# Performance work log

Hardware: AMD Instinct MI355X
Metric: run time of the kernel (lower is better)

The kernel has to match this reference:

```python
import jax, jax.numpy as jnp
import numpy as np

B, H, W, C = 8, 28, 28, 1024
NH = 16
HD = C // NH
HID = 4 * C
BC = C // 2
SCALE = HD ** -0.5
EPS_LN = 1e-5   # nn.LayerNorm default
EPS_CLN = 1e-6  # detectron2 LayerNorm default


def layer_norm(x, w, b, eps=EPS_LN):
    m = jnp.mean(x, -1, keepdims=True)
    v = jnp.mean((x - m) ** 2, -1, keepdims=True)
    return (x - m) * jax.lax.rsqrt(v + eps) * w + b


def conv2d(x, w, padding):
    return jax.lax.conv_general_dilated(x, w, (1, 1), padding,
                                        dimension_numbers=("NHWC", "HWIO", "NHWC"))


def rel_table(rel_pos, size):
    # q_size == k_size, so relative index is simply (i - j) + (size - 1)
    idx = jnp.arange(size)[:, None] - jnp.arange(size)[None, :] + (size - 1)
    return rel_pos[idx]  # (size, size, HD)


def setup_inputs() -> dict:
    key = jax.random.key(0)
    ks = jax.random.split(key, 12)
    rn = lambda k, shape, s=0.02: jax.random.normal(k, shape, jnp.float32) * s
    return {
        "x": jax.random.normal(ks[0], (B, H, W, C), jnp.float32),
        "ln1_w": jnp.ones((C,), jnp.float32), "ln1_b": jnp.zeros((C,), jnp.float32),
        "qkv_w": rn(ks[1], (C, 3 * C)), "qkv_b": jnp.zeros((3 * C,), jnp.float32),
        "proj_w": rn(ks[2], (C, C)), "proj_b": jnp.zeros((C,), jnp.float32),
        "rel_pos_h": rn(ks[3], (2 * H - 1, HD)),
        "rel_pos_w": rn(ks[4], (2 * W - 1, HD)),
        "ln2_w": jnp.ones((C,), jnp.float32), "ln2_b": jnp.zeros((C,), jnp.float32),
        "mlp_w1": rn(ks[5], (C, HID)), "mlp_b1": jnp.zeros((HID,), jnp.float32),
        "mlp_w2": rn(ks[6], (HID, C)), "mlp_b2": jnp.zeros((C,), jnp.float32),
        "conv1_w": rn(ks[7], (1, 1, C, BC)),
        "cln1_w": jnp.ones((BC,), jnp.float32), "cln1_b": jnp.zeros((BC,), jnp.float32),
        "conv2_w": rn(ks[8], (3, 3, BC, BC)),
        "cln2_w": jnp.ones((BC,), jnp.float32), "cln2_b": jnp.zeros((BC,), jnp.float32),
        "conv3_w": rn(ks[9], (1, 1, BC, C)),
        "cln3_w": jnp.ones((C,), jnp.float32), "cln3_b": jnp.zeros((C,), jnp.float32),
    }


def _attention(h, qkv_w, qkv_b, proj_w, proj_b, rel_pos_h, rel_pos_w):
    # h: (B, N, C) with N = H*W
    Bq, N, _ = h.shape
    qkv = (h @ qkv_w + qkv_b).reshape(Bq, N, 3, NH, HD)
    q, k, v = jnp.moveaxis(qkv, 2, 0)          # each (B, N, NH, HD)
    q = jnp.swapaxes(q, 1, 2)                  # (B, NH, N, HD)
    k = jnp.swapaxes(k, 1, 2)
    v = jnp.swapaxes(v, 1, 2)
    attn = jnp.einsum("bhqd,bhkd->bhqk", q * SCALE, k)  # (B, NH, N, N)
    # decomposed relative position bias (uses UNscaled q, as in torch source)
    Rh = rel_table(rel_pos_h, H)               # (H, H, HD)
    Rw = rel_table(rel_pos_w, W)               # (W, W, HD)
    rq = q.reshape(Bq, NH, H, W, HD)
    rel_h = jnp.einsum("bnhwd,hkd->bnhwk", rq, Rh)  # (B, NH, H, W, H)
    rel_w = jnp.einsum("bnhwd,wkd->bnhwk", rq, Rw)  # (B, NH, H, W, W)
    attn = (attn.reshape(Bq, NH, H, W, H, W)
            + rel_h[..., :, None] + rel_w[..., None, :]).reshape(Bq, NH, N, N)
    attn = jax.nn.softmax(attn, axis=-1)
    out = jnp.einsum("bhqk,bhkd->bhqd", attn, v)     # (B, NH, N, HD)
    out = jnp.swapaxes(out, 1, 2).reshape(Bq, N, C)
    return out @ proj_w + proj_b


def reference(x, ln1_w, ln1_b, qkv_w, qkv_b, proj_w, proj_b, rel_pos_h, rel_pos_w,
              ln2_w, ln2_b, mlp_w1, mlp_b1, mlp_w2, mlp_b2,
              conv1_w, cln1_w, cln1_b, conv2_w, cln2_w, cln2_b,
              conv3_w, cln3_w, cln3_b):
    Bq = x.shape[0]
    N = H * W
    xt = x.reshape(Bq, N, C)
    shortcut = xt
    h = layer_norm(xt, ln1_w, ln1_b)
    a = _attention(h, qkv_w, qkv_b, proj_w, proj_b, rel_pos_h, rel_pos_w)
    xt = shortcut + a
    h2 = layer_norm(xt, ln2_w, ln2_b)
    mlp = jax.nn.gelu(h2 @ mlp_w1 + mlp_b1, approximate=False) @ mlp_w2 + mlp_b2
    xt = xt + mlp
    y = xt.reshape(Bq, H, W, C)
    # residual bottleneck conv block (NHWC; detectron2 LN == per-pixel channel LN)
    o = conv2d(y, conv1_w, "VALID")
    o = jax.nn.gelu(layer_norm(o, cln1_w, cln1_b, EPS_CLN), approximate=False)
    o = conv2d(o, conv2_w, "SAME")
    o = jax.nn.gelu(layer_norm(o, cln2_w, cln2_b, EPS_CLN), approximate=False)
    o = conv2d(o, conv3_w, "VALID")
    o = layer_norm(o, cln3_w, cln3_b, EPS_CLN)
    return y + o
```

## Files before the change

### kernel.cpp

```cpp
#include <hip/hip_runtime.h>
#include <hip/hip_bf16.h>

#define DI __device__ __forceinline__

typedef short bf16x8 __attribute__((ext_vector_type(8)));
typedef float f32x4 __attribute__((ext_vector_type(4)));

constexpr int BB = 8, CC = 1024, NHEAD = 16, HD = 64, HIDC = 4096, BCC = 512;
constexpr int NT = 784;
constexpr int MROWS = BB * NT;
constexpr float ATT_SCALE = 0.125f;

DI short f2bf(float f) {
    unsigned u = __builtin_bit_cast(unsigned, f);
    u = u + 0x7FFFu + ((u >> 16) & 1u);
    return (short)(u >> 16);
}
DI float bf2f(short h) {
    unsigned u = ((unsigned)(unsigned short)h) << 16;
    return __builtin_bit_cast(float, u);
}
DI float gelu_f(float x) { return 0.5f * x * (1.0f + erff(x * 0.70710678118654752f)); }

DI void gload16(const void* g, void* l) {
    __builtin_amdgcn_global_load_lds(
        (const __attribute__((address_space(1))) void*)g,
        (__attribute__((address_space(3))) void*)l, 16, 0, 0);
}

__global__ __launch_bounds__(256)
void cvt_t_kernel(const float* __restrict__ in, short* __restrict__ out, int K, int N) {
    __shared__ short t[64][68];
    const int k0 = blockIdx.y * 64, n0 = blockIdx.x * 64;
    const int tid = threadIdx.x;
    const int r = tid >> 4, c4 = (tid & 15) << 2;
    #pragma unroll
    for (int rr = 0; rr < 64; rr += 16) {
        float4 v = *(const float4*)(in + (size_t)(k0 + r + rr) * N + n0 + c4);
        t[r + rr][c4 + 0] = f2bf(v.x); t[r + rr][c4 + 1] = f2bf(v.y);
        t[r + rr][c4 + 2] = f2bf(v.z); t[r + rr][c4 + 3] = f2bf(v.w);
    }
    __syncthreads();
    #pragma unroll
    for (int rr = 0; rr < 64; rr += 16) {
        int nrow = r + rr;
        short4 o;
        o.x = t[c4 + 0][nrow]; o.y = t[c4 + 1][nrow];
        o.z = t[c4 + 2][nrow]; o.w = t[c4 + 3][nrow];
        *(short4*)(out + (size_t)(n0 + nrow) * K + k0 + c4) = o;
    }
}

__global__ void cvt_tables_kernel(const float* __restrict__ rph, const float* __restrict__ rpw,
                                  short* __restrict__ rhb, short* __restrict__ rwb) {
    int i = blockIdx.x * 256 + threadIdx.x;
    if (i < 3520) rhb[i] = f2bf(rph[i]);
    else if (i < 7040) rwb[i - 3520] = f2bf(rpw[i - 3520]);
}

template<bool GELU_, bool RESID, bool OUTBF>
__global__ void ln_kernel(const float* __restrict__ in, const float* __restrict__ gw,
                          const float* __restrict__ gb, const float* __restrict__ resid,
                          void* __restrict__ outv, int C, float eps) {
    const int row = blockIdx.x;
    const int tid = threadIdx.x;
    const float* x = in + (size_t)row * C;
    const int c4 = C >> 2;
    float s = 0.f, s2 = 0.f;
    for (int i = tid; i < c4; i += 256) {
        float4 v = ((const float4*)x)[i];
        s += v.x + v.y + v.z + v.w;
        s2 += v.x * v.x + v.y * v.y + v.z * v.z + v.w * v.w;
    }
    for (int off = 32; off; off >>= 1) { s += __shfl_xor(s, off); s2 += __shfl_xor(s2, off); }
    __shared__ float sa[4], sb[4], stats[2];
    int wid = tid >> 6;
    if ((tid & 63) == 0) { sa[wid] = s; sb[wid] = s2; }
    __syncthreads();
    if (tid == 0) {
        float S = sa[0] + sa[1] + sa[2] + sa[3];
        float S2 = sb[0] + sb[1] + sb[2] + sb[3];
        float mean = S / C;
        float var = S2 / C - mean * mean;
        stats[0] = mean; stats[1] = rsqrtf(var + eps);
    }
    __syncthreads();
    const float mean = stats[0], rstd = stats[1];
    for (int i = tid; i < c4; i += 256) {
        float4 v = ((const float4*)x)[i];
        float4 w4 = ((const float4*)gw)[i];
        float4 b4 = ((const float4*)gb)[i];
        float o[4] = { (v.x - mean) * rstd * w4.x + b4.x,
                       (v.y - mean) * rstd * w4.y + b4.y,
                       (v.z - mean) * rstd * w4.z + b4.z,
                       (v.w - mean) * rstd * w4.w + b4.w };
        if (GELU_) {
            #pragma unroll
            for (int j = 0; j < 4; j++) o[j] = gelu_f(o[j]);
        }
        if (RESID) {
            float4 r4 = ((const float4*)(resid + (size_t)row * C))[i];
            o[0] += r4.x; o[1] += r4.y; o[2] += r4.z; o[3] += r4.w;
        }
        if (OUTBF) {
            short4 ov; ov.x = f2bf(o[0]); ov.y = f2bf(o[1]); ov.z = f2bf(o[2]); ov.w = f2bf(o[3]);
            ((short4*)((short*)outv + (size_t)row * C))[i] = ov;
        } else {
            float4 ov; ov.x = o[0]; ov.y = o[1]; ov.z = o[2]; ov.w = o[3];
            ((float4*)((float*)outv + (size_t)row * C))[i] = ov;
        }
    }
}

template<bool OUTBF, bool HASB, bool ACTG, bool HASR, bool IMC, bool DUAL>
__global__ __launch_bounds__(256)
void gemm_kernel(const short* __restrict__ A, const short* __restrict__ Bt,
                 const float* __restrict__ bias, const float* __restrict__ resid,
                 void* __restrict__ outv, short* __restrict__ out2,
                 int M, int N, int K, const short* __restrict__ zg) {
    __shared__ __align__(16) short As[128 * 32];
    __shared__ __align__(16) short Bs[128 * 32];
    const int tid = threadIdx.x;
    const int nwg = gridDim.x * gridDim.y;
    const int orig = blockIdx.y * gridDim.x + blockIdx.x;
    const int qq = nwg >> 3, rr8 = nwg & 7;
    const int xcd = orig & 7, loc = orig >> 3;
    const int wg = (xcd < rr8 ? xcd * (qq + 1) : rr8 * (qq + 1) + (xcd - rr8) * qq) + loc;
    const int m0 = (wg / gridDim.x) * 128, n0 = (wg % gridDim.x) * 128;
    const int lane = tid & 63, wid = tid >> 6;
    const int wr = (wid >> 1) * 64, wc = (wid & 1) * 64;
    const int lr = lane & 15, lkb = lane >> 4;

    const int srow = lane >> 2;
    const int schunk = lane & 3;

    const short* aptr[2];
    const short* bptr[2];
    short* adst[2]; short* bdst[2];
    int ihh[2], iww[2], ioff[2];
    const short* ibase[2];

    #pragma unroll
    for (int i = 0; i < 2; i++) {
        int seg = wid * 2 + i;
        int row = seg * 16 + srow;
        int c = schunk ^ (row & 3);
        adst[i] = As + seg * 512;
        bdst[i] = Bs + seg * 512;
        bptr[i] = Bt + (size_t)(n0 + row) * K + c * 8;
        if (!IMC) {
            aptr[i] = A + (size_t)(m0 + row) * K + c * 8;
        } else {
            int m = m0 + row;
            int bimg = m / 784, rem = m - bimg * 784;
            ihh[i] = rem / 28; iww[i] = rem - (rem / 28) * 28;
            ibase[i] = A + (size_t)bimg * 784 * 512;
            ioff[i] = c * 8;
        }
    }

    f32x4 acc[4][4];
    #pragma unroll
    for (int i = 0; i < 4; i++)
        #pragma unroll
        for (int j = 0; j < 4; j++) acc[i][j] = f32x4{0.f, 0.f, 0.f, 0.f};

    const int pc = (lkb ^ (lr & 3)) << 3;
    const int nkt = K >> 5;
    for (int kt = 0; kt < nkt; ++kt) {
        if (!IMC) {
            #pragma unroll
            for (int i = 0; i < 2; i++) {
                gload16(aptr[i] + kt * 32, adst[i]);
                gload16(bptr[i] + kt * 32, bdst[i]);
            }
        } else {
            int segk = kt >> 4;
            int ky = segk / 3, kx = segk - ky * 3;
            int ccb = (kt & 15) << 5;
            #pragma unroll
            for (int i = 0; i < 2; i++) {
                int ih = ihh[i] + ky - 1, iw = iww[i] + kx - 1;
                bool ok = (ih >= 0) & (ih < 28) & (iw >= 0) & (iw < 28);
                const short* s = ok ? ibase[i] + ((size_t)(ih * 28 + iw) * 512 + ccb + ioff[i]) : zg;
                gload16(s, adst[i]);
                gload16(bptr[i] + kt * 32, bdst[i]);
            }
        }
        __syncthreads();
        bf16x8 af[4], bfv[4];
        #pragma unroll
        for (int mt = 0; mt < 4; mt++) af[mt] = *(const bf16x8*)&As[(wr + mt * 16 + lr) * 32 + pc];
        #pragma unroll
        for (int nt = 0; nt < 4; nt++) bfv[nt] = *(const bf16x8*)&Bs[(wc + nt * 16 + lr) * 32 + pc];
        #pragma unroll
        for (int mt = 0; mt < 4; mt++)
            #pragma unroll
            for (int nt = 0; nt < 4; nt++)
                acc[mt][nt] = __builtin_amdgcn_mfma_f32_16x16x32_bf16(af[mt], bfv[nt], acc[mt][nt], 0, 0, 0);
        __syncthreads();
    }
    const int ro = (lane >> 4) << 2;
    #pragma unroll
    for (int mt = 0; mt < 4; mt++) {
        #pragma unroll
        for (int nt = 0; nt < 4; nt++) {
            int col = n0 + wc + nt * 16 + lr;
            float bv = HASB ? bias[col] : 0.0f;
            #pragma unroll
            for (int j = 0; j < 4; j++) {
                int row = m0 + wr + mt * 16 + ro + j;
                float v = acc[mt][nt][j] + bv;
                if (ACTG) v = gelu_f(v);
                size_t oi = (size_t)row * N + col;
                if (HASR) v += resid[oi];
                if (OUTBF) ((short*)outv)[oi] = f2bf(v);
                else       ((float*)outv)[oi] = v;
                if (DUAL)  out2[oi] = f2bf(v);
            }
        }
    }
}

__global__ __launch_bounds__(64)
void relpos_mfma_kernel(const short* __restrict__ qkv, const short* __restrict__ rhb,
                        const short* __restrict__ rwb, float* __restrict__ relh,
                        float* __restrict__ relw) {
    const int p = blockIdx.x;
    const int bh = blockIdx.y;
    const int mode = blockIdx.z;
    const int bimg = bh >> 4, nh = bh & 15;
    const int lane = threadIdx.x;
    const int lr = lane & 15, lkb = lane >> 4;
    const short* rb = mode ? rwb : rhb;
    float* outp = mode ? relw : relh;

    bf16x8 afr[2][2];
    #pragma unroll
    for (int mt = 0; mt < 2; mt++) {
        int kh = mt * 16 + lr;
        int sr = p - kh + 27;
        sr = sr < 0 ? 0 : (sr > 54 ? 54 : sr);
        #pragma unroll
        for (int ks = 0; ks < 2; ks++)
            afr[mt][ks] = *(const bf16x8*)(rb + sr * 64 + ks * 32 + lkb * 8);
    }
    bf16x8 bfq[2][2];
    #pragma unroll
    for (int nt = 0; nt < 2; nt++) {
        int cc = nt * 16 + lr;
        int nlin = mode ? (cc * 28 + p) : (p * 28 + cc);
        if (nlin > 783) nlin = 783;
        const short* qp = qkv + (size_t)(bimg * 784 + nlin) * 3072 + nh * 64;
        #pragma unroll
        for (int ks = 0; ks < 2; ks++)
            bfq[nt][ks] = *(const bf16x8*)(qp + ks * 32 + lkb * 8);
    }
    f32x4 acc[2][2];
    #pragma unroll
    for (int i = 0; i < 2; i++)
        #pragma unroll
        for (int j = 0; j < 2; j++) acc[i][j] = f32x4{0.f, 0.f, 0.f, 0.f};
    #pragma unroll
    for (int ks = 0; ks < 2; ks++)
        #pragma unroll
        for (int mt = 0; mt < 2; mt++)
            #pragma unroll
            for (int nt = 0; nt < 2; nt++)
                acc[mt][nt] = __builtin_amdgcn_mfma_f32_16x16x32_bf16(afr[mt][ks], bfq[nt][ks], acc[mt][nt], 0, 0, 0);
    const int ro = lkb << 2;
    #pragma unroll
    for (int nt = 0; nt < 2; nt++) {
        int cc = nt * 16 + lr;
        if (cc < 28) {
            int nlin = mode ? (cc * 28 + p) : (p * 28 + cc);
            float* o = outp + ((size_t)bh * 784 + nlin) * 28;
            *(f32x4*)(o + ro) = acc[0][nt];
            if (ro < 12) *(f32x4*)(o + 16 + ro) = acc[1][nt];
        }
    }
}

__global__ __launch_bounds__(64)
void attn_kernel(const short* __restrict__ qkv, const float* __restrict__ relh,
                 const float* __restrict__ relw, short* __restrict__ outp) {
    __shared__ __align__(16) short Vt[64 * 40];
    __shared__ __align__(16) short Pl[16 * 40];
    __shared__ float relS[16 * 56];
    const int qt = blockIdx.x;
    const int bh = blockIdx.y;
    const int bimg = bh >> 4, nh = bh & 15;
    const int lane = threadIdx.x;
    const int lr = lane & 15, lk = (lane >> 4) * 8;
    const int kg = lane & 7, dblk = lane >> 3;

    for (int idx = lane; idx < 16 * 56; idx += 64) {
        int qq = idx / 56, j = idx - qq * 56;
        int n = qt * 16 + qq;
        relS[idx] = (j < 28) ? relh[((size_t)bh * 784 + n) * 28 + j]
                             : relw[((size_t)bh * 784 + n) * 28 + (j - 28)];
    }
    bf16x8 bq[2];
    {
        int tok = bimg * 784 + qt * 16 + lr;
        const short* qp = qkv + (size_t)tok * 3072 + nh * 64;
        bq[0] = *(const bf16x8*)(qp + lk);
        bq[1] = *(const bf16x8*)(qp + 32 + lk);
    }
    f32x4 oacc[4];
    #pragma unroll
    for (int i = 0; i < 4; i++) oacc[i] = f32x4{0.f, 0.f, 0.f, 0.f};
    float m_run = -1e30f, l_run = 0.0f;
    __syncthreads();

    for (int kt = 0; kt < 25; ++kt) {
        {
            bf16x8 vv[4];
            #pragma unroll
            for (int r = 0; r < 4; r++) {
                int key = kt * 32 + kg * 4 + r;
                if (key < 784)
                    vv[r] = *(const bf16x8*)(qkv + (size_t)(bimg * 784 + key) * 3072 + 2048 + nh * 64 + dblk * 8);
                else
                    vv[r] = bf16x8{0,0,0,0,0,0,0,0};
            }
            #pragma unroll
            for (int j = 0; j < 8; j++) {
                short4 s4; s4.x = vv[0][j]; s4.y = vv[1][j]; s4.z = vv[2][j]; s4.w = vv[3][j];
                *(short4*)&Vt[(dblk * 8 + j) * 40 + kg * 4] = s4;
            }
        }
        f32x4 sacc[2];
        sacc[0] = f32x4{0.f, 0.f, 0.f, 0.f}; sacc[1] = f32x4{0.f, 0.f, 0.f, 0.f};
        #pragma unroll
        for (int mb = 0; mb < 2; mb++) {
            int key = kt * 32 + mb * 16 + lr;
            bf16x8 ak0 = {0,0,0,0,0,0,0,0}, ak1 = {0,0,0,0,0,0,0,0};
            if (key < 784) {
                const short* kp = qkv + (size_t)(bimg * 784 + key) * 3072 + 1024 + nh * 64;
                ak0 = *(const bf16x8*)(kp + lk);
                ak1 = *(const bf16x8*)(kp + 32 + lk);
            }
            sacc[mb] = __builtin_amdgcn_mfma_f32_16x16x32_bf16(ak0, bq[0], sacc[mb], 0, 0, 0);
            sacc[mb] = __builtin_amdgcn_mfma_f32_16x16x32_bf16(ak1, bq[1], sacc[mb], 0, 0, 0);
        }
        float sv[8];
        #pragma unroll
        for (int mb = 0; mb < 2; mb++)
            #pragma unroll
            for (int j = 0; j < 4; j++) {
                int keyloc = mb * 16 + ((lane >> 4) << 2) + j;
                int key = kt * 32 + keyloc;
                float v;
                if (key < 784) {
                    int h2 = key / 28, w2 = key - (key / 28) * 28;
                    v = sacc[mb][j] * ATT_SCALE + relS[lr * 56 + h2] + relS[lr * 56 + 28 + w2];
                } else v = -1e30f;
                sv[mb * 4 + j] = v;
            }
        float mt_ = sv[0];
        #pragma unroll
        for (int i = 1; i < 8; i++) mt_ = fmaxf(mt_, sv[i]);
        mt_ = fmaxf(mt_, __shfl_xor(mt_, 16));
        mt_ = fmaxf(mt_, __shfl_xor(mt_, 32));
        float mnew = fmaxf(m_run, mt_);
        float corr = __expf(m_run - mnew);
        float psum = 0.f;
        #pragma unroll
        for (int mb = 0; mb < 2; mb++)
            #pragma unroll
            for (int j = 0; j < 4; j++) {
                int keyloc = mb * 16 + ((lane >> 4) << 2) + j;
                float pz = __expf(sv[mb * 4 + j] - mnew);
                psum += pz;
                Pl[lr * 40 + keyloc] = f2bf(pz);
            }
        psum += __shfl_xor(psum, 16);
        psum += __shfl_xor(psum, 32);
        l_run = l_run * corr + psum;
        m_run = mnew;
        #pragma unroll
        for (int db = 0; db < 4; db++) {
            f32x4 t = oacc[db];
            t[0] *= corr; t[1] *= corr; t[2] *= corr; t[3] *= corr;
            oacc[db] = t;
        }
        __syncthreads();
        bf16x8 pb = *(const bf16x8*)&Pl[lr * 40 + lk];
        #pragma unroll
        for (int db = 0; db < 4; db++) {
            bf16x8 av = *(const bf16x8*)&Vt[(db * 16 + lr) * 40 + lk];
            oacc[db] = __builtin_amdgcn_mfma_f32_16x16x32_bf16(av, pb, oacc[db], 0, 0, 0);
        }
        __syncthreads();
    }
    const float inv = 1.0f / l_run;
    const int tok = bimg * 784 + qt * 16 + lr;
    short* op = outp + (size_t)tok * 1024 + nh * 64;
    #pragma unroll
    for (int db = 0; db < 4; db++)
        #pragma unroll
        for (int j = 0; j < 4; j++) {
            int d = db * 16 + ((lane >> 4) << 2) + j;
            op[d] = f2bf(oacc[db][j] * inv);
        }
}

extern "C" void kernel_launch(void* const* d_in, const int* in_sizes, int n_in,
                              void* d_out, int out_size, void* d_ws, size_t ws_size,
                              hipStream_t stream) {
    const float* x      = (const float*)d_in[0];
    const float* ln1w   = (const float*)d_in[1];
    const float* ln1b   = (const float*)d_in[2];
    const float* qkvw   = (const float*)d_in[3];
    const float* qkvbia = (const float*)d_in[4];
    const float* projw  = (const float*)d_in[5];
    const float* projb  = (const float*)d_in[6];
    const float* rph    = (const float*)d_in[7];
    const float* rpw    = (const float*)d_in[8];
    const float* ln2w   = (const float*)d_in[9];
    const float* ln2b   = (const float*)d_in[10];
    const float* m1w    = (const float*)d_in[11];
    const float* m1b    = (const float*)d_in[12];
    const float* m2w    = (const float*)d_in[13];
    const float* m2b    = (const float*)d_in[14];
    const float* c1w    = (const float*)d_in[15];
    const float* cl1w   = (const float*)d_in[16];
    const float* cl1b   = (const float*)d_in[17];
    const float* c2w    = (const float*)d_in[18];
    const float* cl2w   = (const float*)d_in[19];
    const float* cl2b   = (const float*)d_in[20];
    const float* c3w    = (const float*)d_in[21];
    const float* cl3w   = (const float*)d_in[22];
    const float* cl3b   = (const float*)d_in[23];
    float* out = (float*)d_out;

    char* base = (char*)d_ws;
    size_t off = 0;
    auto alloc = [&](size_t bytes) -> char* {
        char* p = base + off;
        off = (off + bytes + 255) & ~(size_t)255;
        return p;
    };
    short* wq  = (short*)alloc((size_t)3072 * 1024 * 2);
    short* wp  = (short*)alloc((size_t)1024 * 1024 * 2);
    short* w1  = (short*)alloc((size_t)4096 * 1024 * 2);
    short* w2  = (short*)alloc((size_t)1024 * 4096 * 2);
    short* wc1 = (short*)alloc((size_t)512 * 1024 * 2);
    short* wc2 = (short*)alloc((size_t)512 * 4608 * 2);
    short* wc3 = (short*)alloc((size_t)1024 * 512 * 2);
    short* hbuf = (short*)alloc((size_t)MROWS * 1024 * 2);
    short* qkvb = (short*)alloc((size_t)MROWS * 3072 * 2);
    float* relh = (float*)alloc((size_t)128 * 784 * 28 * 4);
    float* relw = (float*)alloc((size_t)128 * 784 * 28 * 4);
    float* xt   = (float*)alloc((size_t)MROWS * 1024 * 4);
    short* hid  = (short*)alloc((size_t)MROWS * 4096 * 2);
    float* yf   = (float*)alloc((size_t)MROWS * 1024 * 4);
    short* zg   = (short*)alloc(256);
    short* rhb  = (short*)alloc(3520 * 2);
    short* rwb  = (short*)alloc(3520 * 2);
    (void)relw; (void)ws_size; (void)in_sizes; (void)n_in; (void)out_size;

    float* o1f  = (float*)hid;
    short* o1g  = (short*)((char*)hid + (size_t)MROWS * 512 * 4);
    float* o2f  = (float*)((char*)o1g + (size_t)MROWS * 512 * 2);
    short* o2g  = (short*)((char*)o2f + (size_t)MROWS * 512 * 4);
    float* o3f  = (float*)qkvb;
    short* ybf  = (short*)relh;

    hipMemsetAsync(zg, 0, 256, stream);

    auto cvtT = [&](const float* src, short* dst, int K, int N) {
        cvt_t_kernel<<<dim3(N / 64, K / 64), 256, 0, stream>>>(src, dst, K, N);
    };
    cvtT(qkvw, wq, 1024, 3072);
    cvtT(projw, wp, 1024, 1024);
    cvtT(m1w, w1, 1024, 4096);
    cvtT(m2w, w2, 4096, 1024);
    cvtT(c1w, wc1, 1024, 512);
    cvtT(c2w, wc2, 4608, 512);
    cvtT(c3w, wc3, 512, 1024);
    cvt_tables_kernel<<<28, 256, 0, stream>>>(rph, rpw, rhb, rwb);

    ln_kernel<false, false, true><<<MROWS, 256, 0, stream>>>(x, ln1w, ln1b, nullptr, hbuf, 1024, 1e-5f);
    gemm_kernel<true, true, false, false, false, false><<<dim3(24, 49), 256, 0, stream>>>(
        hbuf, wq, qkvbia, nullptr, qkvb, nullptr, MROWS, 3072, 1024, zg);
    relpos_mfma_kernel<<<dim3(28, 128, 2), 64, 0, stream>>>(qkvb, rhb, rwb, relh, relw);
    attn_kernel<<<dim3(49, 128), 64, 0, stream>>>(qkvb, relh, relw, hbuf);
    gemm_kernel<false, true, false, true, false, false><<<dim3(8, 49), 256, 0, stream>>>(
        hbuf, wp, projb, x, xt, nullptr, MROWS, 1024, 1024, zg);
    ln_kernel<false, false, true><<<MROWS, 256, 0, stream>>>(xt, ln2w, ln2b, nullptr, hbuf, 1024, 1e-5f);
    gemm_kernel<true, true, true, false, false, false><<<dim3(32, 49), 256, 0, stream>>>(
        hbuf, w1, m1b, nullptr, hid, nullptr, MROWS, 4096, 1024, zg);
    gemm_kernel<false, true, false, true, false, true><<<dim3(8, 49), 256, 0, stream>>>(
        hid, w2, m2b, xt, yf, ybf, MROWS, 1024, 4096, zg);
    gemm_kernel<false, false, false, false, false, false><<<dim3(4, 49), 256, 0, stream>>>(
        ybf, wc1, nullptr, nullptr, o1f, nullptr, MROWS, 512, 1024, zg);
    ln_kernel<true, false, true><<<MROWS, 256, 0, stream>>>(o1f, cl1w, cl1b, nullptr, o1g, 512, 1e-6f);
    gemm_kernel<false, false, false, false, true, false><<<dim3(4, 49), 256, 0, stream>>>(
        o1g, wc2, nullptr, nullptr, o2f, nullptr, MROWS, 512, 4608, zg);
    ln_kernel<true, false, true><<<MROWS, 256, 0, stream>>>(o2f, cl2w, cl2b, nullptr, o2g, 512, 1e-6f);
    gemm_kernel<false, false, false, false, false, false><<<dim3(8, 49), 256, 0, stream>>>(
        o2g, wc3, nullptr, nullptr, o3f, nullptr, MROWS, 1024, 512, zg);
    ln_kernel<false, true, false><<<MROWS, 256, 0, stream>>>(o3f, cl3w, cl3b, yf, out, 1024, 1e-6f);
}
```

Measured before the change: 836.0 us.

## Share K/V tiles across four query waves in attention, add lazy softmax rescale

The attention kernel now runs 256 threads per block, with four waves each handling 16 queries. K and V tiles are staged once in shared memory (K through swizzled async loads) and reused by all four waves, instead of each 64-thread block reading K and V from global memory on its own. A lazy rescale skips the running-max correction while the new max stays within a fixed threshold of the old one, which removes exp and multiply work. Risks are the extra barriers, clamped padding rows in the last block, and a possible bf16 range issue because exp values can grow to e^8 before rescaling.

```diff
diff --git a/kernel.cpp b/kernel.cpp
--- a/kernel.cpp
+++ b/kernel.cpp
@@ -281,80 +281,80 @@
     }
 }
 
-__global__ __launch_bounds__(64)
+__global__ __launch_bounds__(256)
 void attn_kernel(const short* __restrict__ qkv, const float* __restrict__ relh,
                  const float* __restrict__ relw, short* __restrict__ outp) {
-    __shared__ __align__(16) short Vt[64 * 40];
-    __shared__ __align__(16) short Pl[16 * 40];
-    __shared__ float relS[16 * 56];
-    const int qt = blockIdx.x;
+    constexpr int VSTR = 34;
+    __shared__ __align__(16) short Ks[32 * 64];
+    __shared__ __align__(16) short Vt[64 * VSTR];
+    __shared__ __align__(16) short Pl[4][16 * 40];
+    __shared__ float relS[4][16 * 57];
+    const int qb = blockIdx.x;
     const int bh = blockIdx.y;
     const int bimg = bh >> 4, nh = bh & 15;
-    const int lane = threadIdx.x;
-    const int lr = lane & 15, lk = (lane >> 4) * 8;
-    const int kg = lane & 7, dblk = lane >> 3;
+    const int tid = threadIdx.x;
+    const int lane = tid & 63, wid = tid >> 6;
+    const int lr = lane & 15, lkb = lane >> 4;
+    const int lk = lkb * 8;
+    const int qw0 = qb * 64 + wid * 16;
 
     for (int idx = lane; idx < 16 * 56; idx += 64) {
         int qq = idx / 56, j = idx - qq * 56;
-        int n = qt * 16 + qq;
-        relS[idx] = (j < 28) ? relh[((size_t)bh * 784 + n) * 28 + j]
-                             : relw[((size_t)bh * 784 + n) * 28 + (j - 28)];
-    }
-    bf16x8 bq[2];
+        int n = qw0 + qq; if (n > 783) n = 783;
+        relS[wid][qq * 57 + j] = (j < 28) ? relh[((size_t)bh * 784 + n) * 28 + j]
+                                          : relw[((size_t)bh * 784 + n) * 28 + (j - 28)];
+    }
+    bf16x8 bq0, bq1;
     {
-        int tok = bimg * 784 + qt * 16 + lr;
-        const short* qp = qkv + (size_t)tok * 3072 + nh * 64;
-        bq[0] = *(const bf16x8*)(qp + lk);
-        bq[1] = *(const bf16x8*)(qp + 32 + lk);
+        int tok = qw0 + lr; if (tok > 783) tok = 783;
+        const short* qp = qkv + (size_t)(bimg * 784 + tok) * 3072 + nh * 64;
+        bq0 = *(const bf16x8*)(qp + lk);
+        bq1 = *(const bf16x8*)(qp + 32 + lk);
     }
     f32x4 oacc[4];
     #pragma unroll
     for (int i = 0; i < 4; i++) oacc[i] = f32x4{0.f, 0.f, 0.f, 0.f};
     float m_run = -1e30f, l_run = 0.0f;
-    __syncthreads();
+
+    const int krow = tid >> 3, kcp = tid & 7;
+    const int kclog = kcp ^ (krow & 7);
+    short* kdst = Ks + wid * 512;
+    const int vkey = tid & 31, vdb = tid >> 5;
+    const int kq4 = lkb << 2;
 
     for (int kt = 0; kt < 25; ++kt) {
+        const int k0 = kt * 32;
         {
-            bf16x8 vv[4];
-            #pragma unroll
-            for (int r = 0; r < 4; r++) {
-                int key = kt * 32 + kg * 4 + r;
-                if (key < 784)
-                    vv[r] = *(const bf16x8*)(qkv + (size_t)(bimg * 784 + key) * 3072 + 2048 + nh * 64 + dblk * 8);
-                else
-                    vv[r] = bf16x8{0,0,0,0,0,0,0,0};
-            }
-            #pragma unroll
-            for (int j = 0; j < 8; j++) {
-                short4 s4; s4.x = vv[0][j]; s4.y = vv[1][j]; s4.z = vv[2][j]; s4.w = vv[3][j];
-                *(short4*)&Vt[(dblk * 8 + j) * 40 + kg * 4] = s4;
-            }
-        }
+            int key = k0 + krow; if (key > 783) key = 783;
+            gload16(qkv + (size_t)(bimg * 784 + key) * 3072 + 1024 + nh * 64 + kclog * 8, kdst);
+        }
+        {
+            int key = k0 + vkey; if (key > 783) key = 783;
+            bf16x8 vv = *(const bf16x8*)(qkv + (size_t)(bimg * 784 + key) * 3072 + 2048 + nh * 64 + vdb * 8);
+            #pragma unroll
+            for (int j = 0; j < 8; j++) Vt[(vdb * 8 + j) * VSTR + vkey] = vv[j];
+        }
+        __syncthreads();
         f32x4 sacc[2];
         sacc[0] = f32x4{0.f, 0.f, 0.f, 0.f}; sacc[1] = f32x4{0.f, 0.f, 0.f, 0.f};
         #pragma unroll
         for (int mb = 0; mb < 2; mb++) {
-            int key = kt * 32 + mb * 16 + lr;
-            bf16x8 ak0 = {0,0,0,0,0,0,0,0}, ak1 = {0,0,0,0,0,0,0,0};
-            if (key < 784) {
-                const short* kp = qkv + (size_t)(bimg * 784 + key) * 3072 + 1024 + nh * 64;
-                ak0 = *(const bf16x8*)(kp + lk);
-                ak1 = *(const bf16x8*)(kp + 32 + lk);
-            }
-            sacc[mb] = __builtin_amdgcn_mfma_f32_16x16x32_bf16(ak0, bq[0], sacc[mb], 0, 0, 0);
-            sacc[mb] = __builtin_amdgcn_mfma_f32_16x16x32_bf16(ak1, bq[1], sacc[mb], 0, 0, 0);
+            int row = mb * 16 + lr;
+            bf16x8 ak0 = *(const bf16x8*)&Ks[row * 64 + ((lkb ^ (row & 7)) << 3)];
+            bf16x8 ak1 = *(const bf16x8*)&Ks[row * 64 + (((4 + lkb) ^ (row & 7)) << 3)];
+            sacc[mb] = __builtin_amdgcn_mfma_f32_16x16x32_bf16(ak0, bq0, sacc[mb], 0, 0, 0);
+            sacc[mb] = __builtin_amdgcn_mfma_f32_16x16x32_bf16(ak1, bq1, sacc[mb], 0, 0, 0);
         }
         float sv[8];
         #pragma unroll
         for (int mb = 0; mb < 2; mb++)
             #pragma unroll
             for (int j = 0; j < 4; j++) {
-                int keyloc = mb * 16 + ((lane >> 4) << 2) + j;
-                int key = kt * 32 + keyloc;
+                int key = k0 + mb * 16 + kq4 + j;
                 float v;
                 if (key < 784) {
                     int h2 = key / 28, w2 = key - (key / 28) * 28;
-                    v = sacc[mb][j] * ATT_SCALE + relS[lr * 56 + h2] + relS[lr * 56 + 28 + w2];
+                    v = sacc[mb][j] * ATT_SCALE + relS[wid][lr * 57 + h2] + relS[wid][lr * 57 + 28 + w2];
                 } else v = -1e30f;
                 sv[mb * 4 + j] = v;
             }
@@ -363,47 +363,58 @@
         for (int i = 1; i < 8; i++) mt_ = fmaxf(mt_, sv[i]);
         mt_ = fmaxf(mt_, __shfl_xor(mt_, 16));
         mt_ = fmaxf(mt_, __shfl_xor(mt_, 32));
-        float mnew = fmaxf(m_run, mt_);
-        float corr = __expf(m_run - mnew);
-        float psum = 0.f;
-        #pragma unroll
-        for (int mb = 0; mb < 2; mb++)
+        if (__all(mt_ - m_run <= 8.0f)) {
+            float psum = 0.f;
+            #pragma unroll
+            for (int i = 0; i < 8; i++) {
+                float pz = __expf(sv[i] - m_run);
+                psum += pz;
+                Pl[wid][lr * 40 + ((i >> 2) * 16 + kq4 + (i & 3))] = f2bf(pz);
+            }
+            psum += __shfl_xor(psum, 16);
+            psum += __shfl_xor(psum, 32);
+            l_run += psum;
+        } else {
+            float mnew = fmaxf(m_run, mt_);
+            float corr = __expf(m_run - mnew);
+            float psum = 0.f;
+            #pragma unroll
+            for (int i = 0; i < 8; i++) {
+                float pz = __expf(sv[i] - mnew);
+                psum += pz;
+                Pl[wid][lr * 40 + ((i >> 2) * 16 + kq4 + (i & 3))] = f2bf(pz);
+            }
+            psum += __shfl_xor(psum, 16);
+            psum += __shfl_xor(psum, 32);
+            l_run = l_run * corr + psum;
+            m_run = mnew;
+            #pragma unroll
+            for (int db = 0; db < 4; db++) {
+                f32x4 t = oacc[db];
+                t[0] *= corr; t[1] *= corr; t[2] *= corr; t[3] *= corr;
+                oacc[db] = t;
+            }
+        }
+        bf16x8 pb = *(const bf16x8*)&Pl[wid][lr * 40 + lk];
+        #pragma unroll
+        for (int db = 0; db < 4; db++) {
+            bf16x8 av = *(const bf16x8*)&Vt[(db * 16 + lr) * VSTR + lk];
+            oacc[db] = __builtin_amdgcn_mfma_f32_16x16x32_bf16(av, pb, oacc[db], 0, 0, 0);
+        }
+        __syncthreads();
+    }
+    const float inv = 1.0f / l_run;
+    const int tok = qw0 + lr;
+    if (tok < 784) {
+        short* op = outp + (size_t)(bimg * 784 + tok) * 1024 + nh * 64;
+        #pragma unroll
+        for (int db = 0; db < 4; db++)
             #pragma unroll
             for (int j = 0; j < 4; j++) {
-                int keyloc = mb * 16 + ((lane >> 4) << 2) + j;
-                float pz = __expf(sv[mb * 4 + j] - mnew);
-                psum += pz;
-                Pl[lr * 40 + keyloc] = f2bf(pz);
-            }
-        psum += __shfl_xor(psum, 16);
-        psum += __shfl_xor(psum, 32);
-        l_run = l_run * corr + psum;
-        m_run = mnew;
-        #pragma unroll
-        for (int db = 0; db < 4; db++) {
-            f32x4 t = oacc[db];
-            t[0] *= corr; t[1] *= corr; t[2] *= corr; t[3] *= corr;
-            oacc[db] = t;
-        }
-        __syncthreads();
-        bf16x8 pb = *(const bf16x8*)&Pl[lr * 40 + lk];
-        #pragma unroll
-        for (int db = 0; db < 4; db++) {
-            bf16x8 av = *(const bf16x8*)&Vt[(db * 16 + lr) * 40 + lk];
-            oacc[db] = __builtin_amdgcn_mfma_f32_16x16x32_bf16(av, pb, oacc[db], 0, 0, 0);
-        }
-        __syncthreads();
-    }
-    const float inv = 1.0f / l_run;
-    const int tok = bimg * 784 + qt * 16 + lr;
-    short* op = outp + (size_t)tok * 1024 + nh * 64;
-    #pragma unroll
-    for (int db = 0; db < 4; db++)
-        #pragma unroll
-        for (int j = 0; j < 4; j++) {
-            int d = db * 16 + ((lane >> 4) << 2) + j;
-            op[d] = f2bf(oacc[db][j] * inv);
-        }
+                int d = db * 16 + kq4 + j;
+                op[d] = f2bf(oacc[db][j] * inv);
+            }
+    }
 }
 
 extern "C" void kernel_launch(void* const* d_in, const int* in_sizes, int n_in,
@@ -486,7 +497,7 @@
     gemm_kernel<true, true, false, false, false, false><<<dim3(24, 49), 256, 0, stream>>>(
         hbuf, wq, qkvbia, nullptr, qkvb, nullptr, MROWS, 3072, 1024, zg);
     relpos_mfma_kernel<<<dim3(28, 128, 2), 64, 0, stream>>>(qkvb, rhb, rwb, relh, relw);
-    attn_kernel<<<dim3(49, 128), 64, 0, stream>>>(qkvb, relh, relw, hbuf);
+    attn_kernel<<<dim3(13, 128), 256, 0, stream>>>(qkvb, relh, relw, hbuf);
     gemm_kernel<false, true, false, true, false, false><<<dim3(8, 49), 256, 0, stream>>>(
         hbuf, wp, projb, x, xt, nullptr, MROWS, 1024, 1024, zg);
     ln_kernel<false, false, true><<<MROWS, 256, 0, stream>>>(xt, ln2w, ln2b, nullptr, hbuf, 1024, 1e-5f);
```

Result: faster. 773.7 us (-7.5%).
